# Performance work log

Hardware: AMD Instinct MI355X
Metric: run time of the kernel (lower is better)

## Reference

```python
import jax, jax.numpy as jnp
import numpy as np

N_NODES = 50000
N_EDGES = 800000
N_FEAT = 16
N_BASIS = 4
GAMMA = 10.0
R_MAX = 5.0
INV_SQRT2 = 0.7071067811865476


def setup_inputs() -> dict:
    key = jax.random.key(0)
    k1, k2, k3, k4 = jax.random.split(key, 4)
    pos = jax.random.normal(k1, (N_NODES, 3), dtype=jnp.float32)
    node_features = jax.random.normal(k2, (N_NODES, N_FEAT), dtype=jnp.float32)
    # build edges with no self-loops: dst = (src + 1 + r) % N, r in [0, N-2]
    src = jax.random.randint(k3, (N_EDGES,), 0, N_NODES)
    r = jax.random.randint(k4, (N_EDGES,), 0, N_NODES - 1)
    dst = (src + 1 + r) % N_NODES
    edge_idx = jnp.stack([src, dst], axis=0).astype(jnp.int64)
    return {"pos": pos, "node_features": node_features, "edge_idx": edge_idx}


def _gaussian_basis(d):
    # d: [E] -> [E, N_BASIS]
    centers = jnp.linspace(0.0, R_MAX, N_BASIS, dtype=d.dtype)
    return jnp.exp(-GAMMA * (d[:, None] - centers[None, :]) ** 2)


def _pos_to_rep(v):
    # v: [N, 3, C] cartesian along axis -2 -> complex spherical l=1 basis,
    # returned as stacked (real, imag): [2, N, 3, C]
    x, y, z = v[..., 0, :], v[..., 1, :], v[..., 2, :]
    zero = jnp.zeros_like(z)
    real = jnp.stack([x * INV_SQRT2, z, -x * INV_SQRT2], axis=-2)
    imag = jnp.stack([-y * INV_SQRT2, zero, -y * INV_SQRT2], axis=-2)
    return jnp.stack([real, imag], axis=0)


def reference(pos, node_features, edge_idx):
    src, dst = edge_idx[0], edge_idx[1]
    disp = pos[dst] - pos[src]                      # [E, 3]
    dist = jnp.linalg.norm(disp, axis=-1)           # [E]
    bf = _gaussian_basis(dist)                      # [E, B]
    unit = disp / dist[:, None]                     # [E, 3]
    nf = node_features[dst]                         # [E, F]
    # outer products: [E, 3, B, F]
    edge_vals = (unit[:, :, None, None] * bf[:, None, :, None]
                 * nf[:, None, None, :])
    edge_vals = edge_vals.reshape(edge_vals.shape[0], 3, N_BASIS * N_FEAT)
    node_vecs = jax.ops.segment_sum(edge_vals, src, num_segments=N_NODES)  # [N,3,C]
    return _pos_to_rep(node_vecs)
```

## Files before the change

### kernel.cpp

```cpp
#include <hip/hip_runtime.h>

#define N_FEAT 16
#define N_BASIS 4
#define GAMMA 10.0f
#define R_MAX 5.0f
#define INV_SQRT2 0.70710678118654752f

#define BUCKET 32
#define CAP 768
#define MAXB 2048
#define SC_BLOCK 512
#define SC_EDGES 4096
#define ACC_BLOCK 512
#define ACC_GRID 1024

#define SLOTCAP 1280
#define ROWSTRIDE 1288

#define KC      (-GAMMA * 1.4426950408889634f)
#define CKD     (R_MAX / (N_BASIS - 1))

#if __has_builtin(__builtin_amdgcn_exp2f)
#define EXP2(x) __builtin_amdgcn_exp2f(x)
#else
#define EXP2(x) exp2f(x)
#endif

typedef _Float16 half8 __attribute__((ext_vector_type(8)));
typedef float f32x4 __attribute__((ext_vector_type(4)));

__global__ void bucket_scatter_kernel(const int* __restrict__ src,
                                      const int* __restrict__ dst,
                                      const float* __restrict__ pos,
                                      const float* __restrict__ nfeat,
                                      float4* __restrict__ pos4,
                                      _Float16* __restrict__ nf16,
                                      int* __restrict__ gcursor,
                                      int* __restrict__ sorted,
                                      int n_edges, int nbuck, int n_nodes) {
    __shared__ int h[MAXB];
    __shared__ int cur[MAXB];
    __shared__ int gbase[MAXB];
    __shared__ int pay[SC_EDGES];

    int t = threadIdx.x;

    {
        int i = blockIdx.x * SC_BLOCK + t;
        if (i < n_nodes) {
            pos4[i] = make_float4(pos[3 * i], pos[3 * i + 1], pos[3 * i + 2], 0.0f);
            const float4* nfs = (const float4*)(nfeat + ((size_t)i << 4));
            half8 lo, hi;
            float4 v0 = nfs[0], v1 = nfs[1], v2 = nfs[2], v3 = nfs[3];
            lo[0] = (_Float16)v0.x; lo[1] = (_Float16)v0.y;
            lo[2] = (_Float16)v0.z; lo[3] = (_Float16)v0.w;
            lo[4] = (_Float16)v1.x; lo[5] = (_Float16)v1.y;
            lo[6] = (_Float16)v1.z; lo[7] = (_Float16)v1.w;
            hi[0] = (_Float16)v2.x; hi[1] = (_Float16)v2.y;
            hi[2] = (_Float16)v2.z; hi[3] = (_Float16)v2.w;
            hi[4] = (_Float16)v3.x; hi[5] = (_Float16)v3.y;
            hi[6] = (_Float16)v3.z; hi[7] = (_Float16)v3.w;
            half8* dst16 = (half8*)(nf16 + ((size_t)i << 4));
            dst16[0] = lo;
            dst16[1] = hi;
        }
    }

    int base_e = blockIdx.x * SC_EDGES;
    int nloc = n_edges - base_e;
    if (nloc > SC_EDGES) nloc = SC_EDGES;

    for (int i = t; i < nbuck; i += SC_BLOCK) h[i] = 0;
    __syncthreads();

    unsigned pk[8];
    bool ok[8];
#pragma unroll
    for (int r = 0; r < 8; ++r) {
        int i = t + r * SC_BLOCK;
        ok[r] = (i < nloc);
        unsigned s = ok[r] ? (unsigned)src[base_e + i] : 0u;
        unsigned d = ok[r] ? (unsigned)dst[base_e + i] : 0u;
        pk[r] = (s << 16) | d;
        if (ok[r]) atomicAdd(&h[s >> 5], 1);
    }
    __syncthreads();

    if (t < 64) {
        int run = 0;
        for (int base = 0; base < nbuck; base += 64) {
            int i = base + t;
            int v = (i < nbuck) ? h[i] : 0;
            int incl = v;
            for (int off = 1; off < 64; off <<= 1) {
                int y = __shfl_up(incl, off, 64);
                if (t >= off) incl += y;
            }
            if (i < nbuck) h[i] = run + incl - v;
            run += __shfl(incl, 63, 64);
        }
    }
    __syncthreads();
    for (int i = t; i < nbuck; i += SC_BLOCK) cur[i] = h[i];
    __syncthreads();

#pragma unroll
    for (int r = 0; r < 8; ++r) {
        if (ok[r]) {
            int b = (int)(pk[r] >> 21);
            int p = atomicAdd(&cur[b], 1);
            pay[p] = (int)pk[r];
        }
    }
    __syncthreads();

    for (int b = t; b < nbuck; b += SC_BLOCK) {
        int c = cur[b] - h[b];
        gbase[b] = (c > 0) ? atomicAdd(&gcursor[b], c) : 0;
    }
    __syncthreads();

    for (int i = t; i < nloc; i += SC_BLOCK) {
        unsigned P = (unsigned)pay[i];
        int b = (int)(P >> 21);
        int idx = gbase[b] + (i - h[b]);
        if (idx < CAP) sorted[b * CAP + idx] = (int)P;
    }
}

__global__ __launch_bounds__(ACC_BLOCK) void accumulate_kernel(
        const float4* __restrict__ pos4,
        const _Float16* __restrict__ nf16,
        const int* __restrict__ sorted,
        const int* __restrict__ gcursor,
        float* __restrict__ out,
        int n_nodes, int nbuck) {
    __shared__ _Float16 a_lds[12 * ROWSTRIDE];
    __shared__ unsigned short slot_dst[SLOTCAP];
    __shared__ int cnt[BUCKET];
    __shared__ int soff[BUCKET];
    __shared__ int curs[BUCKET];
    __shared__ float4 spos[BUCKET];

    int t = threadIdx.x;
    int w = t >> 6;
    int lane = t & 63;
    int q = lane >> 4;
    int f = lane & 15;
    int arow = (f < 12) ? f : 11;

    for (int b = blockIdx.x; b < nbuck; b += ACC_GRID) {
        int nbase = b << 5;
        int ecnt = gcursor[b];
        if (ecnt > CAP) ecnt = CAP;
        const int* seg = sorted + b * CAP;

        {
            int4 z4 = make_int4(0, 0, 0, 0);
            int4* az = (int4*)a_lds;
            for (int i = t; i < 1932; i += ACC_BLOCK) az[i] = z4;
            int4* sz = (int4*)slot_dst;
            if (t < 160) sz[t] = z4;
        }
        if (t < BUCKET) {
            cnt[t] = 0;
            int gn = nbase + t;
            spos[t] = (gn < n_nodes) ? pos4[gn] : make_float4(0.f, 0.f, 0.f, 0.f);
        }
        __syncthreads();

        for (int i = t; i < ecnt; i += ACC_BLOCK)
            atomicAdd(&cnt[((unsigned)seg[i] >> 16) & 31], 1);
        __syncthreads();

        if (t < BUCKET) {
            int deg = cnt[t];
            int pad = (deg + 31) & ~31;
            int incl = pad;
            for (int o2 = 1; o2 < BUCKET; o2 <<= 1) {
                int y = __shfl_up(incl, o2, 64);
                if (t >= o2) incl += y;
            }
            int excl = incl - pad;
            soff[t] = excl;
            curs[t] = excl;
        }
        __syncthreads();

        if (ecnt > 0) {
            int ecm1 = ecnt - 1;
            int i0 = t, i1 = t + ACC_BLOCK;
            bool v0 = (i0 < ecnt), v1 = (i1 < ecnt);
            unsigned E0 = (unsigned)seg[min(i0, ecm1)];
            unsigned E1 = (unsigned)seg[min(i1, ecm1)];
            int d0 = E0 & 0xFFFF, d1 = E1 & 0xFFFF;
            float4 pd0 = pos4[d0];
            float4 pd1 = pos4[d1];
            int sl0 = (E0 >> 16) & 31, sl1 = (E1 >> 16) & 31;
            int p0 = v0 ? atomicAdd(&curs[sl0], 1) : SLOTCAP;
            int p1 = v1 ? atomicAdd(&curs[sl1], 1) : SLOTCAP;

#define STAGE(P, SL, D, PD)                                            \
            if ((P) < SLOTCAP) {                                       \
                float4 ps = spos[SL];                                  \
                float dx = (PD).x - ps.x, dy = (PD).y - ps.y,          \
                      dz = (PD).z - ps.z;                              \
                float r2 = dx * dx + dy * dy + dz * dz;                \
                float inv = __builtin_amdgcn_rsqf(r2);                 \
                float dist = r2 * inv;                                 \
                float ux = dx * inv, uy = dy * inv, uz = dz * inv;     \
                slot_dst[P] = (unsigned short)(D);                     \
                _Float16* ap = a_lds + (P);                            \
                _Pragma("unroll")                                      \
                for (int kk = 0; kk < N_BASIS; ++kk) {                 \
                    float ck = (float)kk * CKD;                        \
                    float tt = dist - ck;                              \
                    float bb = EXP2(tt * tt * KC);                     \
                    ap[kk * ROWSTRIDE]       = (_Float16)(ux * bb);    \
                    ap[(4 + kk) * ROWSTRIDE] = (_Float16)(uy * bb);    \
                    ap[(8 + kk) * ROWSTRIDE] = (_Float16)(uz * bb);    \
                }                                                      \
            }
            { STAGE(p0, sl0, d0, pd0); }
            if (v1) { STAGE(p1, sl1, d1, pd1); }
#undef STAGE
        }
        __syncthreads();

        const _Float16* abase = &a_lds[arow * ROWSTRIDE];
#pragma unroll
        for (int half = 0; half < 2; ++half) {
            int nA = (w << 2) + (half << 1);
            int nB = nA + 1;
            int baseA = min(soff[nA], SLOTCAP - 32);
            int baseB = min(soff[nB], SLOTCAP - 32);
            int kA = baseA + (q << 3), kB = baseB + (q << 3);

            half8 aA = *(const half8*)&abase[kA];
            half8 aB = *(const half8*)&abase[kB];
            const unsigned short* dpA = &slot_dst[kA];
            const unsigned short* dpB = &slot_dst[kB];
            half8 bA, bB;
#pragma unroll
            for (int j = 0; j < 8; ++j) bA[j] = nf16[((int)dpA[j] << 4) + f];
#pragma unroll
            for (int j = 0; j < 8; ++j) bB[j] = nf16[((int)dpB[j] << 4) + f];

            f32x4 CA = {0.f, 0.f, 0.f, 0.f};
            f32x4 CB = {0.f, 0.f, 0.f, 0.f};
            CA = __builtin_amdgcn_mfma_f32_16x16x32_f16(aA, bA, CA, 0, 0, 0);
            CB = __builtin_amdgcn_mfma_f32_16x16x32_f16(aB, bB, CB, 0, 0, 0);

            int ntA = min((cnt[nA] + 31) >> 5, (SLOTCAP - baseA) >> 5);
            for (int tile = 1; tile < ntA; ++tile) {
                int k0 = baseA + (tile << 5) + (q << 3);
                half8 a = *(const half8*)&abase[k0];
                const unsigned short* dp = &slot_dst[k0];
                half8 bf;
#pragma unroll
                for (int j = 0; j < 8; ++j) bf[j] = nf16[((int)dp[j] << 4) + f];
                CA = __builtin_amdgcn_mfma_f32_16x16x32_f16(a, bf, CA, 0, 0, 0);
            }
            int ntB = min((cnt[nB] + 31) >> 5, (SLOTCAP - baseB) >> 5);
            for (int tile = 1; tile < ntB; ++tile) {
                int k0 = baseB + (tile << 5) + (q << 3);
                half8 a = *(const half8*)&abase[k0];
                const unsigned short* dp = &slot_dst[k0];
                half8 bf;
#pragma unroll
                for (int j = 0; j < 8; ++j) bf[j] = nf16[((int)dp[j] << 4) + f];
                CB = __builtin_amdgcn_mfma_f32_16x16x32_f16(a, bf, CB, 0, 0, 0);
            }

#define EPI(NL, C)                                                     \
            {                                                          \
                int gn = nbase + (NL);                                 \
                if (gn < n_nodes) {                                    \
                    float* re = out + (size_t)gn * 192;                \
                    float* im = re + (size_t)n_nodes * 192;            \
                    _Pragma("unroll")                                  \
                    for (int r = 0; r < 4; ++r) {                      \
                        float v = (C)[r];                              \
                        int o1 = r * 16 + f;                           \
                        if (q == 0) {                                  \
                            float xs = v * INV_SQRT2;                  \
                            re[o1] = xs;                               \
                            re[128 + o1] = -xs;                        \
                        } else if (q == 1) {                           \
                            float ys = -v * INV_SQRT2;                 \
                            im[o1] = ys;                               \
                            im[128 + o1] = ys;                         \
                        } else if (q == 2) {                           \
                            re[64 + o1] = v;                           \
                        } else {                                       \
                            im[64 + o1] = 0.0f;                        \
                        }                                              \
                    }                                                  \
                }                                                      \
            }
            EPI(nA, CA);
            EPI(nB, CB);
#undef EPI
        }
        __syncthreads();
    }
}

extern "C" void kernel_launch(void* const* d_in, const int* in_sizes, int n_in,
                              void* d_out, int out_size, void* d_ws, size_t ws_size,
                              hipStream_t stream) {
    const float* pos = (const float*)d_in[0];
    const float* nfeat = (const float*)d_in[1];
    const int* edge_idx = (const int*)d_in[2];

    int n_nodes = in_sizes[0] / 3;
    int n_edges = in_sizes[2] / 2;

    const int* src = edge_idx;
    const int* dst = edge_idx + n_edges;

    float* out = (float*)d_out;
    int nbuck = (n_nodes + BUCKET - 1) >> 5;

    char* ws = (char*)d_ws;
    size_t o = 0;
    auto alloc = [&](size_t bytes) {
        char* p = ws + o;
        o = (o + bytes + 255) & ~(size_t)255;
        return p;
    };
    int* gcursor   = (int*)alloc((size_t)nbuck * 4);
    int* sorted    = (int*)alloc((size_t)nbuck * CAP * 4);
    float4* pos4   = (float4*)alloc((size_t)n_nodes * 16);
    _Float16* nf16 = (_Float16*)alloc((size_t)n_nodes * 32);

    (void)hipMemsetAsync(gcursor, 0, (size_t)nbuck * sizeof(int), stream);

    {
        int grid = (n_edges + SC_EDGES - 1) / SC_EDGES;
        bucket_scatter_kernel<<<grid, SC_BLOCK, 0, stream>>>(src, dst, pos, nfeat,
                                                             pos4, nf16,
                                                             gcursor, sorted,
                                                             n_edges, nbuck, n_nodes);
    }

    {
        int grid = (nbuck < ACC_GRID) ? nbuck : ACC_GRID;
        accumulate_kernel<<<grid, ACC_BLOCK, 0, stream>>>(pos4, nf16, sorted, gcursor,
                                                          out, n_nodes, nbuck);
    }
}
```

Measured before the change: 58.93 us.

## Fuse memset, bucket scatter and accumulate into one cooperative kernel with grid syncs

Replaces the memset plus two kernel launches with a single cooperative kernel. Grid-wide syncs separate the preprocessing/gcursor zeroing, the bucket scatter (now a grid-stride loop over edge chunks), and the accumulation phase. Shared memory is reused across phases through one aliased buffer, and MAXB shrinks so the footprint fits. The intent is to remove launch gaps and the separate memset, at the cost of grid sync overhead and a grid capped by occupancy.

Result: slower. 189.3 us (+221.3%).

```diff
diff --git a/kernel.cpp b/kernel.cpp
--- a/kernel.cpp
+++ b/kernel.cpp
@@ -1,4 +1,7 @@
 #include <hip/hip_runtime.h>
+#include <hip/hip_cooperative_groups.h>
+
+namespace cg = cooperative_groups;
 
 #define N_FEAT 16
 #define N_BASIS 4
@@ -8,11 +11,9 @@
 
 #define BUCKET 32
 #define CAP 768
-#define MAXB 2048
-#define SC_BLOCK 512
+#define MAXB 1600
 #define SC_EDGES 4096
-#define ACC_BLOCK 512
-#define ACC_GRID 1024
+#define BLOCK 512
 
 #define SLOTCAP 1280
 #define ROWSTRIDE 1288
@@ -29,29 +30,29 @@
 typedef _Float16 half8 __attribute__((ext_vector_type(8)));
 typedef float f32x4 __attribute__((ext_vector_type(4)));
 
-__global__ void bucket_scatter_kernel(const int* __restrict__ src,
-                                      const int* __restrict__ dst,
-                                      const float* __restrict__ pos,
-                                      const float* __restrict__ nfeat,
-                                      float4* __restrict__ pos4,
-                                      _Float16* __restrict__ nf16,
-                                      int* __restrict__ gcursor,
-                                      int* __restrict__ sorted,
-                                      int n_edges, int nbuck, int n_nodes) {
-    __shared__ int h[MAXB];
-    __shared__ int cur[MAXB];
-    __shared__ int gbase[MAXB];
-    __shared__ int pay[SC_EDGES];
-
+#define SMEM_BYTES 35584
+
+__global__ __launch_bounds__(BLOCK, 8) void fused_kernel(
+        const int* __restrict__ src, const int* __restrict__ dst,
+        const float* __restrict__ pos, const float* __restrict__ nfeat,
+        float4* __restrict__ pos4, _Float16* __restrict__ nf16,
+        int* __restrict__ gcursor, int* __restrict__ sorted,
+        float* __restrict__ out,
+        int n_edges, int nbuck, int n_nodes, int nchunks) {
+    __shared__ __align__(16) char smem[SMEM_BYTES];
+    __shared__ float4 spos[BUCKET];
+
+    cg::grid_group gg = cg::this_grid();
     int t = threadIdx.x;
 
     {
-        int i = blockIdx.x * SC_BLOCK + t;
-        if (i < n_nodes) {
+        int gtid = blockIdx.x * BLOCK + t;
+        int gstride = gridDim.x * BLOCK;
+        for (int i = gtid; i < n_nodes; i += gstride) {
             pos4[i] = make_float4(pos[3 * i], pos[3 * i + 1], pos[3 * i + 2], 0.0f);
             const float4* nfs = (const float4*)(nfeat + ((size_t)i << 4));
+            float4 v0 = nfs[0], v1 = nfs[1], v2 = nfs[2], v3 = nfs[3];
             half8 lo, hi;
-            float4 v0 = nfs[0], v1 = nfs[1], v2 = nfs[2], v3 = nfs[3];
             lo[0] = (_Float16)v0.x; lo[1] = (_Float16)v0.y;
             lo[2] = (_Float16)v0.z; lo[3] = (_Float16)v0.w;
             lo[4] = (_Float16)v1.x; lo[5] = (_Float16)v1.y;
@@ -60,267 +61,272 @@
             hi[2] = (_Float16)v2.z; hi[3] = (_Float16)v2.w;
             hi[4] = (_Float16)v3.x; hi[5] = (_Float16)v3.y;
             hi[6] = (_Float16)v3.z; hi[7] = (_Float16)v3.w;
-            half8* dst16 = (half8*)(nf16 + ((size_t)i << 4));
-            dst16[0] = lo;
-            dst16[1] = hi;
+            half8* d16 = (half8*)(nf16 + ((size_t)i << 4));
+            d16[0] = lo; d16[1] = hi;
+        }
+        for (int i = gtid; i < nbuck; i += gstride) gcursor[i] = 0;
+    }
+    gg.sync();
+
+    {
+        int* h     = (int*)smem;
+        int* cur   = h + MAXB;
+        int* gbase = cur + MAXB;
+        int* pay   = gbase + MAXB;
+
+        for (int chunk = blockIdx.x; chunk < nchunks; chunk += gridDim.x) {
+            int base_e = chunk * SC_EDGES;
+            int nloc = n_edges - base_e;
+            if (nloc > SC_EDGES) nloc = SC_EDGES;
+
+            for (int i = t; i < nbuck; i += BLOCK) h[i] = 0;
+            __syncthreads();
+
+            unsigned pk[8];
+            bool ok[8];
+#pragma unroll
+            for (int r = 0; r < 8; ++r) {
+                int i = t + r * BLOCK;
+                ok[r] = (i < nloc);
+                unsigned s = ok[r] ? (unsigned)src[base_e + i] : 0u;
+                unsigned d = ok[r] ? (unsigned)dst[base_e + i] : 0u;
+                pk[r] = (s << 16) | d;
+                if (ok[r]) atomicAdd(&h[s >> 5], 1);
+            }
+            __syncthreads();
+
+            if (t < 64) {
+                int run = 0;
+                for (int base = 0; base < nbuck; base += 64) {
+                    int i = base + t;
+                    int v = (i < nbuck) ? h[i] : 0;
+                    int incl = v;
+                    for (int off = 1; off < 64; off <<= 1) {
+                        int y = __shfl_up(incl, off, 64);
+                        if (t >= off) incl += y;
+                    }
+                    if (i < nbuck) h[i] = run + incl - v;
+                    run += __shfl(incl, 63, 64);
+                }
+            }
+            __syncthreads();
+            for (int i = t; i < nbuck; i += BLOCK) cur[i] = h[i];
+            __syncthreads();
+
+#pragma unroll
+            for (int r = 0; r < 8; ++r) {
+                if (ok[r]) {
+                    int b = (int)(pk[r] >> 21);
+                    int p = atomicAdd(&cur[b], 1);
+                    pay[p] = (int)pk[r];
+                }
+            }
+            __syncthreads();
+
+            for (int b = t; b < nbuck; b += BLOCK) {
+                int c = cur[b] - h[b];
+                gbase[b] = (c > 0) ? atomicAdd(&gcursor[b], c) : 0;
+            }
+            __syncthreads();
+
+            for (int i = t; i < nloc; i += BLOCK) {
+                unsigned P = (unsigned)pay[i];
+                int b = (int)(P >> 21);
+                int idx = gbase[b] + (i - h[b]);
+                if (idx < CAP) sorted[b * CAP + idx] = (int)P;
+            }
+            __syncthreads();
         }
     }
-
-    int base_e = blockIdx.x * SC_EDGES;
-    int nloc = n_edges - base_e;
-    if (nloc > SC_EDGES) nloc = SC_EDGES;
-
-    for (int i = t; i < nbuck; i += SC_BLOCK) h[i] = 0;
-    __syncthreads();
-
-    unsigned pk[8];
-    bool ok[8];
-#pragma unroll
-    for (int r = 0; r < 8; ++r) {
-        int i = t + r * SC_BLOCK;
-        ok[r] = (i < nloc);
-        unsigned s = ok[r] ? (unsigned)src[base_e + i] : 0u;
-        unsigned d = ok[r] ? (unsigned)dst[base_e + i] : 0u;
-        pk[r] = (s << 16) | d;
-        if (ok[r]) atomicAdd(&h[s >> 5], 1);
-    }
-    __syncthreads();
-
-    if (t < 64) {
-        int run = 0;
-        for (int base = 0; base < nbuck; base += 64) {
-            int i = base + t;
-            int v = (i < nbuck) ? h[i] : 0;
-            int incl = v;
-            for (int off = 1; off < 64; off <<= 1) {
-                int y = __shfl_up(incl, off, 64);
-                if (t >= off) incl += y;
-            }
-            if (i < nbuck) h[i] = run + incl - v;
-            run += __shfl(incl, 63, 64);
-        }
-    }
-    __syncthreads();
-    for (int i = t; i < nbuck; i += SC_BLOCK) cur[i] = h[i];
-    __syncthreads();
-
-#pragma unroll
-    for (int r = 0; r < 8; ++r) {
-        if (ok[r]) {
-            int b = (int)(pk[r] >> 21);
-            int p = atomicAdd(&cur[b], 1);
-            pay[p] = (int)pk[r];
-        }
-    }
-    __syncthreads();
-
-    for (int b = t; b < nbuck; b += SC_BLOCK) {
-        int c = cur[b] - h[b];
-        gbase[b] = (c > 0) ? atomicAdd(&gcursor[b], c) : 0;
-    }
-    __syncthreads();
-
-    for (int i = t; i < nloc; i += SC_BLOCK) {
-        unsigned P = (unsigned)pay[i];
-        int b = (int)(P >> 21);
-        int idx = gbase[b] + (i - h[b]);
-        if (idx < CAP) sorted[b * CAP + idx] = (int)P;
-    }
-}
-
-__global__ __launch_bounds__(ACC_BLOCK) void accumulate_kernel(
-        const float4* __restrict__ pos4,
-        const _Float16* __restrict__ nf16,
-        const int* __restrict__ sorted,
-        const int* __restrict__ gcursor,
-        float* __restrict__ out,
-        int n_nodes, int nbuck) {
-    __shared__ _Float16 a_lds[12 * ROWSTRIDE];
-    __shared__ unsigned short slot_dst[SLOTCAP];
-    __shared__ int cnt[BUCKET];
-    __shared__ int soff[BUCKET];
-    __shared__ int curs[BUCKET];
-    __shared__ float4 spos[BUCKET];
-
-    int t = threadIdx.x;
-    int w = t >> 6;
-    int lane = t & 63;
-    int q = lane >> 4;
-    int f = lane & 15;
-    int arow = (f < 12) ? f : 11;
-
-    for (int b = blockIdx.x; b < nbuck; b += ACC_GRID) {
-        int nbase = b << 5;
-        int ecnt = gcursor[b];
-        if (ecnt > CAP) ecnt = CAP;
-        const int* seg = sorted + b * CAP;
-
-        {
-            int4 z4 = make_int4(0, 0, 0, 0);
-            int4* az = (int4*)a_lds;
-            for (int i = t; i < 1932; i += ACC_BLOCK) az[i] = z4;
-            int4* sz = (int4*)slot_dst;
-            if (t < 160) sz[t] = z4;
-        }
-        if (t < BUCKET) {
-            cnt[t] = 0;
-            int gn = nbase + t;
-            spos[t] = (gn < n_nodes) ? pos4[gn] : make_float4(0.f, 0.f, 0.f, 0.f);
-        }
-        __syncthreads();
-
-        for (int i = t; i < ecnt; i += ACC_BLOCK)
-            atomicAdd(&cnt[((unsigned)seg[i] >> 16) & 31], 1);
-        __syncthreads();
-
-        if (t < BUCKET) {
-            int deg = cnt[t];
-            int pad = (deg + 31) & ~31;
-            int incl = pad;
-            for (int o2 = 1; o2 < BUCKET; o2 <<= 1) {
-                int y = __shfl_up(incl, o2, 64);
-                if (t >= o2) incl += y;
-            }
-            int excl = incl - pad;
-            soff[t] = excl;
-            curs[t] = excl;
-        }
-        __syncthreads();
-
-        if (ecnt > 0) {
-            int ecm1 = ecnt - 1;
-            int i0 = t, i1 = t + ACC_BLOCK;
-            bool v0 = (i0 < ecnt), v1 = (i1 < ecnt);
-            unsigned E0 = (unsigned)seg[min(i0, ecm1)];
-            unsigned E1 = (unsigned)seg[min(i1, ecm1)];
-            int d0 = E0 & 0xFFFF, d1 = E1 & 0xFFFF;
-            float4 pd0 = pos4[d0];
-            float4 pd1 = pos4[d1];
-            int sl0 = (E0 >> 16) & 31, sl1 = (E1 >> 16) & 31;
-            int p0 = v0 ? atomicAdd(&curs[sl0], 1) : SLOTCAP;
-            int p1 = v1 ? atomicAdd(&curs[sl1], 1) : SLOTCAP;
+    gg.sync();
+
+    {
+        _Float16* a_lds = (_Float16*)smem;
+        unsigned short* sd = (unsigned short*)(smem + 30912);
+        int* cnt  = (int*)(smem + 33472);
+        int* soff = (int*)(smem + 33600);
+        int* curs = (int*)(smem + 33728);
+
+        int w = t >> 6;
+        int lane = t & 63;
+        int q = lane >> 4;
+        int f = lane & 15;
+        int arow = (f < 12) ? f : 11;
+
+        for (int b = blockIdx.x; b < nbuck; b += gridDim.x) {
+            int nbase = b << 5;
+            int ecnt = gcursor[b];
+            if (ecnt > CAP) ecnt = CAP;
+            const int* seg = sorted + b * CAP;
+
+            {
+                int4 z4 = make_int4(0, 0, 0, 0);
+                int4* az = (int4*)a_lds;
+                for (int i = t; i < 1932; i += BLOCK) az[i] = z4;
+                int4* sz = (int4*)sd;
+                if (t < 160) sz[t] = z4;
+            }
+            if (t < BUCKET) {
+                cnt[t] = 0;
+                int gn = nbase + t;
+                spos[t] = (gn < n_nodes) ? pos4[gn] : make_float4(0.f, 0.f, 0.f, 0.f);
+            }
+            __syncthreads();
+
+            for (int i = t; i < ecnt; i += BLOCK)
+                atomicAdd(&cnt[((unsigned)seg[i] >> 16) & 31], 1);
+            __syncthreads();
+
+            if (t < BUCKET) {
+                int deg = cnt[t];
+                int pad = (deg + 31) & ~31;
+                int incl = pad;
+                for (int o2 = 1; o2 < BUCKET; o2 <<= 1) {
+                    int y = __shfl_up(incl, o2, 64);
+                    if (t >= o2) incl += y;
+                }
+                int excl = incl - pad;
+                soff[t] = excl;
+                curs[t] = excl;
+            }
+            __syncthreads();
+
+            if (ecnt > 0) {
+                int ecm1 = ecnt - 1;
+                int i0 = t, i1 = t + BLOCK;
+                bool v0 = (i0 < ecnt), v1 = (i1 < ecnt);
+                unsigned E0 = (unsigned)seg[min(i0, ecm1)];
+                unsigned E1 = (unsigned)seg[min(i1, ecm1)];
+                int d0 = E0 & 0xFFFF, d1 = E1 & 0xFFFF;
+                float4 pd0 = pos4[d0];
+                float4 pd1 = pos4[d1];
+                int sl0 = (E0 >> 16) & 31, sl1 = (E1 >> 16) & 31;
+                int p0 = v0 ? atomicAdd(&curs[sl0], 1) : SLOTCAP;
+                int p1 = v1 ? atomicAdd(&curs[sl1], 1) : SLOTCAP;
 
 #define STAGE(P, SL, D, PD)                                            \
-            if ((P) < SLOTCAP) {                                       \
-                float4 ps = spos[SL];                                  \
-                float dx = (PD).x - ps.x, dy = (PD).y - ps.y,          \
-                      dz = (PD).z - ps.z;                              \
-                float r2 = dx * dx + dy * dy + dz * dz;                \
-                float inv = __builtin_amdgcn_rsqf(r2);                 \
-                float dist = r2 * inv;                                 \
-                float ux = dx * inv, uy = dy * inv, uz = dz * inv;     \
-                slot_dst[P] = (unsigned short)(D);                     \
-                _Float16* ap = a_lds + (P);                            \
-                _Pragma("unroll")                                      \
-                for (int kk = 0; kk < N_BASIS; ++kk) {                 \
-                    float ck = (float)kk * CKD;                        \
-                    float tt = dist - ck;                              \
-                    float bb = EXP2(tt * tt * KC);                     \
-                    ap[kk * ROWSTRIDE]       = (_Float16)(ux * bb);    \
-                    ap[(4 + kk) * ROWSTRIDE] = (_Float16)(uy * bb);    \
-                    ap[(8 + kk) * ROWSTRIDE] = (_Float16)(uz * bb);    \
-                }                                                      \
-            }
-            { STAGE(p0, sl0, d0, pd0); }
-            if (v1) { STAGE(p1, sl1, d1, pd1); }
+                if ((P) < SLOTCAP) {                                   \
+                    float4 ps = spos[SL];                              \
+                    float dx = (PD).x - ps.x, dy = (PD).y - ps.y,      \
+                          dz = (PD).z - ps.z;                          \
+                    float r2 = dx * dx + dy * dy + dz * dz;            \
+                    float inv = __builtin_amdgcn_rsqf(r2);             \
+                    float dist = r2 * inv;                             \
+                    float ux = dx * inv, uy = dy * inv, uz = dz * inv; \
+                    sd[P] = (unsigned short)(D);                       \
+                    _Float16* ap = a_lds + (P);                        \
+                    _Pragma("unroll")                                  \
+                    for (int kk = 0; kk < N_BASIS; ++kk) {             \
+                        float ck = (float)kk * CKD;                    \
+                        float tt = dist - ck;                          \
+                        float bb = EXP2(tt * tt * KC);                 \
+                        ap[kk * ROWSTRIDE]       = (_Float16)(ux * bb);\
+                        ap[(4 + kk) * ROWSTRIDE] = (_Float16)(uy * bb);\
+                        ap[(8 + kk) * ROWSTRIDE] = (_Float16)(uz * bb);\
+                    }                                                  \
+                }
+                { STAGE(p0, sl0, d0, pd0); }
+                if (v1) { STAGE(p1, sl1, d1, pd1); }
 #undef STAGE
-        }
-        __syncthreads();
-
-        const _Float16* abase = &a_lds[arow * ROWSTRIDE];
-#pragma unroll
-        for (int half = 0; half < 2; ++half) {
-            int nA = (w << 2) + (half << 1);
-            int nB = nA + 1;
-            int baseA = min(soff[nA], SLOTCAP - 32);
-            int baseB = min(soff[nB], SLOTCAP - 32);
-            int kA = baseA + (q << 3), kB = baseB + (q << 3);
-
-            half8 aA = *(const half8*)&abase[kA];
-            half8 aB = *(const half8*)&abase[kB];
-            const unsigned short* dpA = &slot_dst[kA];
-            const unsigned short* dpB = &slot_dst[kB];
-            half8 bA, bB;
-#pragma unroll
-            for (int j = 0; j < 8; ++j) bA[j] = nf16[((int)dpA[j] << 4) + f];
-#pragma unroll
-            for (int j = 0; j < 8; ++j) bB[j] = nf16[((int)dpB[j] << 4) + f];
-
-            f32x4 CA = {0.f, 0.f, 0.f, 0.f};
-            f32x4 CB = {0.f, 0.f, 0.f, 0.f};
-            CA = __builtin_amdgcn_mfma_f32_16x16x32_f16(aA, bA, CA, 0, 0, 0);
-            CB = __builtin_amdgcn_mfma_f32_16x16x32_f16(aB, bB, CB, 0, 0, 0);
-
-            int ntA = min((cnt[nA] + 31) >> 5, (SLOTCAP - baseA) >> 5);
-            for (int tile = 1; tile < ntA; ++tile) {
-                int k0 = baseA + (tile << 5) + (q << 3);
-                half8 a = *(const half8*)&abase[k0];
-                const unsigned short* dp = &slot_dst[k0];
-                half8 bf;
-#pragma unroll
-                for (int j = 0; j < 8; ++j) bf[j] = nf16[((int)dp[j] << 4) + f];
-                CA = __builtin_amdgcn_mfma_f32_16x16x32_f16(a, bf, CA, 0, 0, 0);
-            }
-            int ntB = min((cnt[nB] + 31) >> 5, (SLOTCAP - baseB) >> 5);
-            for (int tile = 1; tile < ntB; ++tile) {
-                int k0 = baseB + (tile << 5) + (q << 3);
-                half8 a = *(const half8*)&abase[k0];
-                const unsigned short* dp = &slot_dst[k0];
-                half8 bf;
-#pragma unroll
-                for (int j = 0; j < 8; ++j) bf[j] = nf16[((int)dp[j] << 4) + f];
-                CB = __builtin_amdgcn_mfma_f32_16x16x32_f16(a, bf, CB, 0, 0, 0);
-            }
+            }
+            __syncthreads();
+
+            const _Float16* abase = &a_lds[arow * ROWSTRIDE];
+#pragma unroll
+            for (int hf = 0; hf < 2; ++hf) {
+                int nA = (w << 2) + (hf << 1);
+                int nB = nA + 1;
+                int baseA = min(soff[nA], SLOTCAP - 32);
+                int baseB = min(soff[nB], SLOTCAP - 32);
+                int kA = baseA + (q << 3), kB = baseB + (q << 3);
+
+                half8 aA = *(const half8*)&abase[kA];
+                half8 aB = *(const half8*)&abase[kB];
+                const unsigned short* dpA = &sd[kA];
+                const unsigned short* dpB = &sd[kB];
+                half8 bA, bB;
+#pragma unroll
+                for (int j = 0; j < 8; ++j) bA[j] = nf16[((int)dpA[j] << 4) + f];
+#pragma unroll
+                for (int j = 0; j < 8; ++j) bB[j] = nf16[((int)dpB[j] << 4) + f];
+
+                f32x4 CA = {0.f, 0.f, 0.f, 0.f};
+                f32x4 CB = {0.f, 0.f, 0.f, 0.f};
+                CA = __builtin_amdgcn_mfma_f32_16x16x32_f16(aA, bA, CA, 0, 0, 0);
+                CB = __builtin_amdgcn_mfma_f32_16x16x32_f16(aB, bB, CB, 0, 0, 0);
+
+                int ntA = min((cnt[nA] + 31) >> 5, (SLOTCAP - baseA) >> 5);
+                for (int tile = 1; tile < ntA; ++tile) {
+                    int k0 = baseA + (tile << 5) + (q << 3);
+                    half8 a = *(const half8*)&abase[k0];
+                    const unsigned short* dp = &sd[k0];
+                    half8 bf;
+#pragma unroll
+                    for (int j = 0; j < 8; ++j) bf[j] = nf16[((int)dp[j] << 4) + f];
+                    CA = __builtin_amdgcn_mfma_f32_16x16x32_f16(a, bf, CA, 0, 0, 0);
+                }
+                int ntB = min((cnt[nB] + 31) >> 5, (SLOTCAP - baseB) >> 5);
+                for (int tile = 1; tile < ntB; ++tile) {
+                    int k0 = baseB + (tile << 5) + (q << 3);
+                    half8 a = *(const half8*)&abase[k0];
+                    const unsigned short* dp = &sd[k0];
+                    half8 bf;
+#pragma unroll
+                    for (int j = 0; j < 8; ++j) bf[j] = nf16[((int)dp[j] << 4) + f];
+                    CB = __builtin_amdgcn_mfma_f32_16x16x32_f16(a, bf, CB, 0, 0, 0);
+                }
 
 #define EPI(NL, C)                                                     \
-            {                                                          \
-                int gn = nbase + (NL);                                 \
-                if (gn < n_nodes) {                                    \
-                    float* re = out + (size_t)gn * 192;                \
-                    float* im = re + (size_t)n_nodes * 192;            \
-                    _Pragma("unroll")                                  \
-                    for (int r = 0; r < 4; ++r) {                      \
-                        float v = (C)[r];                              \
-                        int o1 = r * 16 + f;                           \
-                        if (q == 0) {                                  \
-                            float xs = v * INV_SQRT2;                  \
-                            re[o1] = xs;                               \
-                            re[128 + o1] = -xs;                        \
-                        } else if (q == 1) {                           \
-                            float ys = -v * INV_SQRT2;                 \
-                            im[o1] = ys;                               \
-                            im[128 + o1] = ys;                         \
-                        } else if (q == 2) {                           \
-                            re[64 + o1] = v;                           \
-                        } else {                                       \
-                            im[64 + o1] = 0.0f;                        \
+                {                                                      \
+                    int gn = nbase + (NL);                             \
+                    if (gn < n_nodes) {                                \
+                        float* re = out + (size_t)gn * 192;            \
+                        float* im = re + (size_t)n_nodes * 192;        \
+                        _Pragma("unroll")                              \
+                        for (int r = 0; r < 4; ++r) {                  \
+                            float v = (C)[r];                          \
+                            int o1 = r * 16 + f;                       \
+                            if (q == 0) {                              \
+                                float xs = v * INV_SQRT2;              \
+                                re[o1] = xs;                           \
+                                re[128 + o1] = -xs;                    \
+                            } else if (q == 1) {                       \
+                                float ys = -v * INV_SQRT2;             \
+                                im[o1] = ys;                           \
+                                im[128 + o1] = ys;                     \
+                            } else if (q == 2) {                       \
+                                re[64 + o1] = v;                       \
+                            } else {                                   \
+                                im[64 + o1] = 0.0f;                    \
+                            }                                          \
                         }                                              \
                     }                                                  \
-                }                                                      \
-            }
-            EPI(nA, CA);
-            EPI(nB, CB);
+                }
+                EPI(nA, CA);
+                EPI(nB, CB);
 #undef EPI
+            }
+            __syncthreads();
         }
-        __syncthreads();
     }
 }
 
 extern "C" void kernel_launch(void* const* d_in, const int* in_sizes, int n_in,
                               void* d_out, int out_size, void* d_ws, size_t ws_size,
                               hipStream_t stream) {
+    const int* ei = (const int*)d_in[2];
     const float* pos = (const float*)d_in[0];
     const float* nfeat = (const float*)d_in[1];
-    const int* edge_idx = (const int*)d_in[2];
 
     int n_nodes = in_sizes[0] / 3;
     int n_edges = in_sizes[2] / 2;
 
-    const int* src = edge_idx;
-    const int* dst = edge_idx + n_edges;
+    const int* src = ei;
+    const int* dst = ei + n_edges;
 
     float* out = (float*)d_out;
     int nbuck = (n_nodes + BUCKET - 1) >> 5;
+    int nchunks = (n_edges + SC_EDGES - 1) / SC_EDGES;
 
     char* ws = (char*)d_ws;
     size_t o = 0;
@@ -334,19 +340,18 @@
     float4* pos4   = (float4*)alloc((size_t)n_nodes * 16);
     _Float16* nf16 = (_Float16*)alloc((size_t)n_nodes * 32);
 
-    (void)hipMemsetAsync(gcursor, 0, (size_t)nbuck * sizeof(int), stream);
-
-    {
-        int grid = (n_edges + SC_EDGES - 1) / SC_EDGES;
-        bucket_scatter_kernel<<<grid, SC_BLOCK, 0, stream>>>(src, dst, pos, nfeat,
-                                                             pos4, nf16,
-                                                             gcursor, sorted,
-                                                             n_edges, nbuck, n_nodes);
-    }
-
-    {
-        int grid = (nbuck < ACC_GRID) ? nbuck : ACC_GRID;
-        accumulate_kernel<<<grid, ACC_BLOCK, 0, stream>>>(pos4, nf16, sorted, gcursor,
-                                                          out, n_nodes, nbuck);
-    }
+    int occ = 0;
+    (void)hipOccupancyMaxActiveBlocksPerMultiprocessor(&occ, fused_kernel, BLOCK, 0);
+    if (occ < 1) occ = 1;
+    long long g = (long long)occ * 256;
+    int grid = (g > 1024) ? 1024 : (int)g;
+
+    void* args[] = {
+        (void*)&src, (void*)&dst, (void*)&pos, (void*)&nfeat,
+        (void*)&pos4, (void*)&nf16, (void*)&gcursor, (void*)&sorted,
+        (void*)&out, (void*)&n_edges, (void*)&nbuck, (void*)&n_nodes,
+        (void*)&nchunks
+    };
+    (void)hipLaunchCooperativeKernel((void*)fused_kernel, dim3(grid), dim3(BLOCK),
+                                     args, 0, stream);
 }
```
